# Optimization experiments

Hardware: AMD Instinct MI355X
Metric: run time of the kernel (lower is better)

Reference implementation:

```python
import jax, jax.numpy as jnp
import numpy as np
from jax import lax

B, TX, RX, RATE, DIMZ, HID, DIRS = 8192, 32, 32, 2, 64, 128, 2
S, FEAT = 2 * TX, 2 * TX + 1
BN_EPS = 1e-5
GD_STEP = 1e-6   # hardcoded in original forward
GD_ITERS = 10    # hardcoded in original forward


def setup_inputs() -> dict:
    key = jax.random.key(0)
    ks = jax.random.split(key, 9)
    sc = 1.0 / np.sqrt(HID)
    return {
        "y": jax.random.normal(ks[0], (B, 2 * RX), jnp.float32),
        "H": jax.random.normal(ks[1], (B, 2 * RX, 2 * TX), jnp.float32),
        "x_raw": jax.random.randint(ks[2], (B, 2 * TX, 1), 0, 2 ** RATE).astype(jnp.float32),
        "gru_w_ih": jax.random.uniform(ks[3], (DIRS, 3 * HID, FEAT), jnp.float32, -sc, sc),
        "gru_w_hh": jax.random.uniform(ks[4], (DIRS, 3 * HID, HID), jnp.float32, -sc, sc),
        "gru_b_ih": jax.random.uniform(ks[5], (DIRS, 3 * HID), jnp.float32, -sc, sc),
        "gru_b_hh": jax.random.uniform(ks[6], (DIRS, 3 * HID), jnp.float32, -sc, sc),
        "w_Wz": jax.random.normal(ks[7], (DIMZ, DIRS * HID), jnp.float32),
        "w_Wx": jax.random.normal(ks[8], (DIMZ, DIRS * HID), jnp.float32),
        "bn_gamma": jnp.ones((2 * TX,), jnp.float32),
        "bn_beta": jnp.zeros((2 * TX,), jnp.float32),
        "step_size": 1,
        "iterations": 10,
    }


def _gru_dir(x_seq, wih, whh, bih, bhh):
    # x_seq: (S, B, F); PyTorch GRU cell equations
    xg = jnp.einsum('sbf,gf->sbg', x_seq, wih) + bih  # (S, B, 3H)

    def step(h, xg_t):
        hg = h @ whh.T + bhh
        xr, xz, xn = jnp.split(xg_t, 3, axis=-1)
        hr, hz, hn = jnp.split(hg, 3, axis=-1)
        r = jax.nn.sigmoid(xr + hr)
        z = jax.nn.sigmoid(xz + hz)
        n = jnp.tanh(xn + r * hn)
        h = (1.0 - z) * n + z * h
        return h, h

    h0 = jnp.zeros((x_seq.shape[1], whh.shape[1]), x_seq.dtype)
    _, out = lax.scan(step, h0, xg)
    return out  # (S, B, H)


def reference(y, H, x_raw, gru_w_ih, gru_w_hh, gru_b_ih, gru_b_hh,
              w_Wz, w_Wx, bn_gamma, bn_beta, step_size, iterations):
    # Hty: (B, 2tx, 1), HtH: (B, 2tx, 2tx)
    Hty = jnp.einsum('brt,br->bt', H, y)[..., None]
    HtH = jnp.einsum('brt,bru->btu', H, H)

    # BatchNorm1d over channel dim 2tx (stats over batch and last dim)
    feats = jnp.concatenate([HtH, Hty], axis=-1)  # (B, 2tx, 2tx+1)
    mu = feats.mean(axis=(0, 2), keepdims=True)
    var = feats.var(axis=(0, 2), keepdims=True)
    feats = (feats - mu) / jnp.sqrt(var + BN_EPS)
    feats = feats * bn_gamma[None, :, None] + bn_beta[None, :, None]

    # bidirectional GRU over seq dim (seq_len = 2tx)
    x_seq = jnp.transpose(feats, (1, 0, 2))  # (S, B, F)
    fwd = _gru_dir(x_seq, gru_w_ih[0], gru_w_hh[0], gru_b_ih[0], gru_b_hh[0])
    bwd = _gru_dir(x_seq[::-1], gru_w_ih[1], gru_w_hh[1], gru_b_ih[1], gru_b_hh[1])[::-1]
    go = jnp.concatenate([fwd, bwd], axis=-1)  # (S, B, 2H)

    w_z = jnp.transpose(go @ w_Wz.T, (1, 2, 0))  # (B, dim_z, S)
    w_x = jnp.transpose(go @ w_Wx.T, (1, 0, 2))  # (B, S, dim_z)

    x_hat0 = 2.0 * x_raw - (2.0 ** RATE) + 1.0  # QAM symbols
    z0 = w_z @ x_hat0  # (B, dim_z, 1)

    # gradient-descent loop (step_size/iterations args ignored, as in source)
    wxt = jnp.swapaxes(w_x, 1, 2)        # (B, dim_z, 2tx)
    wxt_hty = wxt @ Hty                  # (B, dim_z, 1)
    whhw = wxt @ (HtH @ w_x)             # (B, dim_z, dim_z)
    two_step = 2.0 * GD_STEP

    def gd(zh, _):
        return zh + two_step * (wxt_hty - whhw @ zh), None

    z_hat, _ = lax.scan(gd, z0, None, length=GD_ITERS)
    return w_x @ z_hat  # (B, 2tx, 1)
```

## Files before the change

### kernel.cpp

```cpp
#include <hip/hip_runtime.h>
#include <math.h>


typedef __attribute__((ext_vector_type(8))) short s8v;
typedef __attribute__((ext_vector_type(4))) float f4v;

__device__ __forceinline__ short f2bf(float x) {
  unsigned u = __float_as_uint(x);
  u += 0x7fffu + ((u >> 16) & 1u);
  return (short)(u >> 16);
}
__device__ __forceinline__ float bf2f(short h) {
  return __uint_as_float(((unsigned)(unsigned short)h) << 16);
}
__device__ __forceinline__ void fma4(float4& c, float a, const float4 w) {
  c.x += a*w.x; c.y += a*w.y; c.z += a*w.z; c.w += a*w.w;
}
__device__ __forceinline__ float vget(const float4& v, int i) { return ((const float*)&v)[i]; }

#define MFMA(A, B, C) __builtin_amdgcn_mfma_f32_16x16x32_bf16((A), (B), (C), 0, 0, 0)

__global__ __launch_bounds__(256) void k_feats(
    const float* __restrict__ Hm, const float* __restrict__ y,
    short* __restrict__ fragX, float* __restrict__ htyU, float* __restrict__ bnacc)
{
  __shared__ __align__(16) float Hl[64][68];
  __shared__ float yl[64];
  __shared__ float s1[64], s2[64];
  const int b = blockIdx.x;
  const int tid = threadIdx.x;
  const float* Hb = Hm + (size_t)b*4096;
  for (int i = tid; i < 4096; i += 256) Hl[i>>6][i&63] = Hb[i];
  if (tid < 64) { yl[tid] = y[b*64+tid]; s1[tid] = 0.f; s2[tid] = 0.f; }
  __syncthreads();

  if (tid < 64) {
    float acc = 0.f;
    for (int r = 0; r < 64; ++r) acc += Hl[r][tid]*yl[r];
    htyU[tid*8192 + b] = acc;
    atomicAdd(&s1[tid], acc);
    atomicAdd(&s2[tid], acc*acc);
  }
  const int tg = tid & 15, ug = tid >> 4;
  float4 acc4[4];
  acc4[0]=acc4[1]=acc4[2]=acc4[3]=make_float4(0.f,0.f,0.f,0.f);
  for (int r = 0; r < 64; ++r) {
    const float4 tv = *(const float4*)&Hl[r][4*tg];
    const float4 uv = *(const float4*)&Hl[r][4*ug];
    #pragma unroll
    for (int tt=0;tt<4;++tt) fma4(acc4[tt], vget(tv,tt), uv);
  }
  const int mt   = (b >> 4) & 3;
  const int brow = b & 15;
  const int u0   = 4*ug;
  short* fbase = fragX + (size_t)(b >> 6)*64*8192
               + (mt*2 + (u0 >> 5))*512 + (brow + 16*((u0 >> 3) & 3))*8 + (u0 & 7);
  #pragma unroll
  for (int tt=0;tt<4;++tt) {
    const int t = 4*tg+tt;
    float sv=0.f, sq=0.f;
    short hib[4], lob[4];
    #pragma unroll
    for (int uu=0;uu<4;++uu) {
      const float v = vget(acc4[tt],uu);
      const short hi = f2bf(v);
      hib[uu] = hi; lob[uu] = f2bf(v - bf2f(hi));
      sv += v; sq += v*v;
    }
    short* dst = fbase + (size_t)t*8192;
    *(short4*)dst          = make_short4(hib[0],hib[1],hib[2],hib[3]);
    *(short4*)(dst + 4096) = make_short4(lob[0],lob[1],lob[2],lob[3]);
    sv += __shfl_down(sv,32); sq += __shfl_down(sq,32);
    sv += __shfl_down(sv,16); sq += __shfl_down(sq,16);
    if ((tid & 63) < 16) { atomicAdd(&s1[t], sv); atomicAdd(&s2[t], sq); }
  }
  __syncthreads();
  if (tid < 64) {
    atomicAdd(&bnacc[tid*16],      s1[tid]);
    atomicAdd(&bnacc[(64+tid)*16], s2[tid]);
  }
}

__global__ void k_bnfin(const float* __restrict__ bnacc, const float* __restrict__ gam,
                        const float* __restrict__ bet, float* __restrict__ bnac)
{
  const int t = threadIdx.x;
  if (t < 64) {
    const float inv = 1.f/532480.f;
    const float mu  = bnacc[t*16]*inv;
    const float var = bnacc[(64+t)*16]*inv - mu*mu;
    const float a = gam[t]*rsqrtf(var + 1e-5f);
    bnac[t] = a;
    bnac[64+t] = bet[t] - mu*a;
  }
}

__global__ __launch_bounds__(256) void k_prep(
    const float* __restrict__ wih, const float* __restrict__ whh,
    const float* __restrict__ Wz, const float* __restrict__ Wx,
    short* __restrict__ Wg, short* __restrict__ W2g, float* __restrict__ rowsum)
{
  const int i = blockIdx.x*256 + threadIdx.x;
  if (i < 294912) {
    const int dd = i / 147456, r = i % 147456;
    const int sp = r / 73728, r2 = r % 73728;
    const int chunk = r2 / 512, e = r2 % 512;
    const int lane = e >> 3, ii = e & 7;
    const int nt = chunk / 6, kt = chunk % 6;
    const int n = nt*16 + (lane & 15);
    const int k = kt*32 + (lane >> 4)*8 + ii;
    const float v = (k < 64) ? wih[dd*24960 + n*65 + k]
                             : whh[dd*49152 + n*128 + (k - 64)];
    const short hi = f2bf(v);
    Wg[i] = sp ? f2bf(v - bf2f(hi)) : hi;
  } else if (i < 360448) {
    const int t = i - 294912;
    const int dd = t / 32768, r = t % 32768;
    const int sp = r / 16384, r2 = r % 16384;
    const int chunk = r2 / 512, e = r2 % 512;
    const int lane = e >> 3, ii = e & 7;
    const int nt2 = chunk / 4, kt = chunk % 4;
    const int n2 = nt2*16 + (lane & 15);
    const int k = kt*32 + (lane >> 4)*8 + ii;
    const float v = (n2 < 64) ? Wx[n2*256 + dd*128 + k]
                              : Wz[(n2 - 64)*256 + dd*128 + k];
    const short hi = f2bf(v);
    W2g[t] = sp ? f2bf(v - bf2f(hi)) : hi;
  } else if (i < 361216) {
    const int t = i - 360448;
    const int dd = t / 384, g = t % 384;
    float ssum = 0.f;
    for (int f = 0; f < 65; ++f) ssum += wih[dd*24960 + g*65 + f];
    rowsum[t] = ssum;
  }
}

__global__ __launch_bounds__(512, 2) void k_scan(
    const short* __restrict__ fragX, const float* __restrict__ htyU,
    const float* __restrict__ xraw,
    const short* __restrict__ Wg, const short* __restrict__ W2g,
    const float* __restrict__ bih, const float* __restrict__ bhh,
    const float* __restrict__ rowsum, const float* __restrict__ bnac,
    const float* __restrict__ wih,
    float* __restrict__ wx_out, float* __restrict__ z0_out)
{
  __shared__ __align__(16) short Ax[8192];
  __shared__ __align__(16) short Ah[16384];

  const int tid = threadIdx.x;
  const int l   = tid & 63;
  const int w   = __builtin_amdgcn_readfirstlane(tid >> 6);
  const int tile = blockIdx.x >> 1, d = blockIdx.x & 1;
  const int b0  = tile * 64;
  const int l15 = l & 15, lq = l >> 4;
  const int j   = 16*w + l15;

  const short* Wgd = Wg  + d*147456;
  const short* W2d = W2g + d*32768;
  float* wxo = wx_out + (size_t)d * (8192ull*4096ull);
  float* z0o = z0_out + (size_t)d * (8192ull*64ull);

  s8v BR[6][2], BZ[6][2], BN[6][2], BP[4][2];
  #pragma unroll
  for (int kt = 0; kt < 6; ++kt)
    #pragma unroll
    for (int sp = 0; sp < 2; ++sp) {
      BR[kt][sp] = *(const s8v*)&Wgd[((sp*24 + w     )*6 + kt)*512 + l*8];
      BZ[kt][sp] = *(const s8v*)&Wgd[((sp*24 + 8 + w )*6 + kt)*512 + l*8];
      BN[kt][sp] = *(const s8v*)&Wgd[((sp*24 + 16 + w)*6 + kt)*512 + l*8];
    }
  #pragma unroll
  for (int kt = 0; kt < 4; ++kt)
    #pragma unroll
    for (int sp = 0; sp < 2; ++sp)
      BP[kt][sp] = *(const s8v*)&W2d[((sp*8 + w)*4 + kt)*512 + l*8];

  const float rsR = rowsum[d*384 + j];
  const float rsZ = rowsum[d*384 + 128 + j];
  const float rsN = rowsum[d*384 + 256 + j];
  const float KR  = bih[d*384 + j]       + bhh[d*384 + j];
  const float KZ  = bih[d*384 + 128 + j] + bhh[d*384 + 128 + j];
  const float KN  = bih[d*384 + 256 + j];
  const float BHN = bhh[d*384 + 256 + j];
  const float w64r = wih[d*24960 + j*65 + 64];
  const float w64z = wih[d*24960 + (128 + j)*65 + 64];
  const float w64n = wih[d*24960 + (256 + j)*65 + 64];

  const int hw_base = (j >> 5)*512 + ((j >> 3) & 3)*128 + (j & 7);

  for (int i = tid; i < 16384; i += 512) Ah[i] = 0;

  f4v hprev[4], z0a[4];
  #pragma unroll
  for (int mt = 0; mt < 4; ++mt) { hprev[mt] = (f4v)0.f; z0a[mt] = (f4v)0.f; }

  {
    const int s0 = d ? 63 : 0;
    const short* src = fragX + (size_t)(tile*64 + s0)*8192;
    *(float4*)((char*)Ax + tid*16)        = *(const float4*)((const char*)src + tid*16);
    *(float4*)((char*)Ax + 8192 + tid*16) = *(const float4*)((const char*)src + 8192 + tid*16);
  }
  __syncthreads();

  for (int it = 0; it < 64; ++it) {
    const int s  = d ? 63 - it : it;
    const int sn = (it < 63) ? (d ? s - 1 : s + 1) : s;

    const short* srcn = fragX + (size_t)(tile*64 + sn)*8192;
    const float4 pf0 = *(const float4*)((const char*)srcn + tid*16);
    const float4 pf1 = *(const float4*)((const char*)srcn + 8192 + tid*16);

    const float a_s = bnac[s], c_s = bnac[64 + s];
    const float crK = c_s*rsR + KR;
    const float czK = c_s*rsZ + KZ;
    const float cnK = c_s*rsN + KN;

    #pragma unroll
    for (int mt = 0; mt < 4; ++mt) {
      f4v Crx = (f4v)0.f, Czx = (f4v)0.f, Cnx = (f4v)0.f;
      f4v Crh = (f4v)0.f, Czh = (f4v)0.f, Cnh = (f4v)0.f;
      #pragma unroll
      for (int kt = 0; kt < 2; ++kt) {
        const s8v axh = *(const s8v*)&Ax[mt*1024 + kt*512 + l*8];
        const s8v axl = *(const s8v*)&Ax[4096 + mt*1024 + kt*512 + l*8];
        Crx = MFMA(axh, BR[kt][0], Crx); Crx = MFMA(axh, BR[kt][1], Crx); Crx = MFMA(axl, BR[kt][0], Crx);
        Czx = MFMA(axh, BZ[kt][0], Czx); Czx = MFMA(axh, BZ[kt][1], Czx); Czx = MFMA(axl, BZ[kt][0], Czx);
        Cnx = MFMA(axh, BN[kt][0], Cnx); Cnx = MFMA(axh, BN[kt][1], Cnx); Cnx = MFMA(axl, BN[kt][0], Cnx);
      }
      #pragma unroll
      for (int kh = 0; kh < 4; ++kh) {
        const s8v ahh = *(const s8v*)&Ah[mt*2048 + kh*512 + l*8];
        const s8v ahl = *(const s8v*)&Ah[8192 + mt*2048 + kh*512 + l*8];
        const int kt = 2 + kh;
        Crh = MFMA(ahh, BR[kt][0], Crh); Crh = MFMA(ahh, BR[kt][1], Crh); Crh = MFMA(ahl, BR[kt][0], Crh);
        Czh = MFMA(ahh, BZ[kt][0], Czh); Czh = MFMA(ahh, BZ[kt][1], Czh); Czh = MFMA(ahl, BZ[kt][0], Czh);
        Cnh = MFMA(ahh, BN[kt][0], Cnh); Cnh = MFMA(ahh, BN[kt][1], Cnh); Cnh = MFMA(ahl, BN[kt][0], Cnh);
      }
      f4v av;
      #pragma unroll
      for (int e = 0; e < 4; ++e) av[e] = htyU[s*8192 + b0 + mt*16 + lq*4 + e];
      Crx += av * w64r; Czx += av * w64z; Cnx += av * w64n;
      #pragma unroll
      for (int e = 0; e < 4; ++e) {
        const float rr  = 1.f/(1.f + __expf(-(a_s*Crx[e] + Crh[e] + crK)));
        const float zz  = 1.f/(1.f + __expf(-(a_s*Czx[e] + Czh[e] + czK)));
        const float pre = a_s*Cnx[e] + cnK + rr*(Cnh[e] + BHN);
        const float ax2 = fabsf(pre);
        const float ee  = __expf(-2.f*ax2);
        const float nn  = copysignf((1.f - ee)/(1.f + ee), pre);
        hprev[mt][e] = (1.f - zz)*nn + zz*hprev[mt][e];
      }
    }
    __syncthreads();

    #pragma unroll
    for (int mt = 0; mt < 4; ++mt)
      #pragma unroll
      for (int e = 0; e < 4; ++e) {
        const float hv = hprev[mt][e];
        const short hi = f2bf(hv);
        const int ad = mt*2048 + hw_base + (lq*4 + e)*8;
        Ah[ad] = hi;
        Ah[8192 + ad] = f2bf(hv - bf2f(hi));
      }
    *(float4*)((char*)Ax + tid*16)        = pf0;
    *(float4*)((char*)Ax + 8192 + tid*16) = pf1;
    __syncthreads();

    #pragma unroll
    for (int mt = 0; mt < 4; ++mt) {
      f4v Cp = (f4v)0.f;
      #pragma unroll
      for (int kt = 0; kt < 4; ++kt) {
        const s8v ahh = *(const s8v*)&Ah[mt*2048 + kt*512 + l*8];
        const s8v ahl = *(const s8v*)&Ah[8192 + mt*2048 + kt*512 + l*8];
        Cp = MFMA(ahh, BP[kt][0], Cp);
        Cp = MFMA(ahh, BP[kt][1], Cp);
        Cp = MFMA(ahl, BP[kt][0], Cp);
      }
      if (w < 4) {
        #pragma unroll
        for (int e = 0; e < 4; ++e)
          wxo[(size_t)(b0 + mt*16 + lq*4 + e)*4096 + s*64 + 16*w + l15] = Cp[e];
      } else {
        f4v xh;
        #pragma unroll
        for (int e = 0; e < 4; ++e)
          xh[e] = 2.f*xraw[(b0 + mt*16 + lq*4 + e)*64 + s] - 3.f;
        z0a[mt] += xh * Cp;
      }
    }
  }
  if (w >= 4) {
    #pragma unroll
    for (int mt = 0; mt < 4; ++mt)
      #pragma unroll
      for (int e = 0; e < 4; ++e)
        z0o[(size_t)(b0 + mt*16 + lq*4 + e)*64 + 16*(w-4) + l15] = z0a[mt][e];
  }
}

__global__ __launch_bounds__(256) void k_gd(
    const float* __restrict__ Hm, const float* __restrict__ y,
    const float* __restrict__ wxf, const float* __restrict__ wxb,
    const float* __restrict__ z0f, const float* __restrict__ z0b,
    float* __restrict__ out)
{
  __shared__ __align__(16) float Hl[64][68];
  __shared__ __align__(16) float wx[64][68];
  __shared__ __align__(16) float tmp[64][68];
  __shared__ float yl[64], wh[64], zv[64];
  const int b = blockIdx.x;
  const int tid = threadIdx.x;
  const float* Hb = Hm + (size_t)b*4096;
  for (int i = tid; i < 4096; i += 256) {
    Hl[i>>6][i&63] = Hb[i];
    wx[i>>6][i&63] = wxf[(size_t)b*4096 + i] + wxb[(size_t)b*4096 + i];
  }
  if (tid < 64) {
    yl[tid] = y[b*64+tid];
    zv[tid] = z0f[(size_t)b*64+tid] + z0b[(size_t)b*64+tid];
  }
  __syncthreads();
  const int zq = tid & 15, tq = tid >> 4;
  #pragma unroll
  for (int rr = 0; rr < 4; ++rr) {
    const int r = 4*tq + rr;
    float4 a = make_float4(0.f,0.f,0.f,0.f);
    for (int t = 0; t < 64; ++t) fma4(a, Hl[r][t], *(const float4*)&wx[t][4*zq]);
    *(float4*)&tmp[r][4*zq] = a;
  }
  __syncthreads();
  float (*ww)[68] = Hl;
  #pragma unroll
  for (int ii = 0; ii < 4; ++ii) {
    const int zi = 4*tq + ii;
    float4 a = make_float4(0.f,0.f,0.f,0.f);
    for (int r = 0; r < 64; ++r) fma4(a, tmp[r][zi], *(const float4*)&tmp[r][4*zq]);
    *(float4*)&ww[zi][4*zq] = a;
  }
  if (tid < 64) {
    float acc = 0.f;
    for (int r = 0; r < 64; ++r) acc += tmp[r][tid]*yl[r];
    wh[tid] = acc;
  }
  __syncthreads();
  for (int itr = 0; itr < 10; ++itr) {
    float nz = 0.f;
    if (tid < 64) {
      float mv = 0.f;
      for (int k2 = 0; k2 < 64; ++k2) mv += ww[tid][k2]*zv[k2];
      nz = zv[tid] + 2e-6f*(wh[tid] - mv);
    }
    __syncthreads();
    if (tid < 64) zv[tid] = nz;
    __syncthreads();
  }
  if (tid < 64) {
    float o = 0.f;
    for (int z2 = 0; z2 < 64; ++z2) o += wx[tid][z2]*zv[z2];
    out[(size_t)b*64 + tid] = o;
  }
}

extern "C" void kernel_launch(void* const* d_in, const int* in_sizes, int n_in,
                              void* d_out, int out_size, void* d_ws, size_t ws_size,
                              hipStream_t stream)
{
  const float* y    = (const float*)d_in[0];
  const float* Hm   = (const float*)d_in[1];
  const float* xraw = (const float*)d_in[2];
  const float* wih  = (const float*)d_in[3];
  const float* whh  = (const float*)d_in[4];
  const float* bih  = (const float*)d_in[5];
  const float* bhh  = (const float*)d_in[6];
  const float* Wz   = (const float*)d_in[7];
  const float* Wx   = (const float*)d_in[8];
  const float* gam  = (const float*)d_in[9];
  const float* bet  = (const float*)d_in[10];
  float* out = (float*)d_out;
  float* ws  = (float*)d_ws;

  float* wxf   = ws;
  float* wxb   = wxf + 33554432ull;
  float* z0f   = wxb + 33554432ull;
  float* z0b   = z0f + 524288ull;
  float* htyU  = z0b + 524288ull;
  float* rows  = htyU + 524288ull;
  float* bnacc = rows + 768ull;
  float* bnac  = bnacc + 2048ull;
  short* Wgs   = (short*)(bnac + 128ull);
  short* W2gs  = Wgs + 294912ull;
  short* fragX = W2gs + 65536ull;

  hipMemsetAsync(bnacc, 0, 2048*sizeof(float), stream);
  k_feats <<<8192, 256, 0, stream>>>(Hm, y, fragX, htyU, bnacc);
  k_prep  <<<1412, 256, 0, stream>>>(wih, whh, Wz, Wx, Wgs, W2gs, rows);
  k_bnfin <<<1, 64, 0, stream>>>(bnacc, gam, bet, bnac);
  k_scan  <<<256, 512, 0, stream>>>(fragX, htyU, xraw, Wgs, W2gs,
                                    bih, bhh, rows, bnac, wih, wxf, z0f);
  k_gd    <<<8192, 256, 0, stream>>>(Hm, y, wxf, wxb, z0f, z0b, out);
}
```

Before: 2.103 ms.

## Double-buffer GRU scan LDS tiles and stage per-step scalars in LDS

Splits the input and hidden-state LDS tiles in the recurrent scan kernel into ping-pong buffers. This removes one of the two block-wide barriers per timestep, since writes to the next step's buffer no longer race with reads of the current one. It also preloads the QAM symbols, the Hty column and the BatchNorm coefficients into LDS once, replacing scattered per-step global loads with vectorised LDS reads. The cost is much more LDS per block (about 131KB), which rules out two resident blocks per CU. With this grid size that may not matter.

```diff
diff --git a/kernel.cpp b/kernel.cpp
--- a/kernel.cpp
+++ b/kernel.cpp
@@ -144,8 +144,11 @@
     const float* __restrict__ wih,
     float* __restrict__ wx_out, float* __restrict__ z0_out)
 {
-  __shared__ __align__(16) short Ax[8192];
-  __shared__ __align__(16) short Ah[16384];
+  __shared__ __align__(16) short Axb[16384];
+  __shared__ __align__(16) short Ahb[32768];
+  __shared__ __align__(16) float xl[64][68];
+  __shared__ __align__(16) float htyl[64][68];
+  __shared__ float bna[128];
 
   const int tid = threadIdx.x;
   const int l   = tid & 63;
@@ -188,7 +191,16 @@
 
   const int hw_base = (j >> 5)*512 + ((j >> 3) & 3)*128 + (j & 7);
 
-  for (int i = tid; i < 16384; i += 512) Ah[i] = 0;
+  for (int i = tid; i < 32768; i += 512) Ahb[i] = 0;
+  for (int i = tid; i < 4096; i += 512) {
+    const int bl = i >> 6, s = i & 63;
+    xl[s][bl] = 2.f*xraw[(size_t)(b0 + bl)*64 + s] - 3.f;
+  }
+  for (int i = tid; i < 4096; i += 512) {
+    const int s = i >> 6, bl = i & 63;
+    htyl[s][bl] = htyU[s*8192 + b0 + bl];
+  }
+  if (tid < 128) bna[tid] = bnac[tid];
 
   f4v hprev[4], z0a[4];
   #pragma unroll
@@ -197,8 +209,8 @@
   {
     const int s0 = d ? 63 : 0;
     const short* src = fragX + (size_t)(tile*64 + s0)*8192;
-    *(float4*)((char*)Ax + tid*16)        = *(const float4*)((const char*)src + tid*16);
-    *(float4*)((char*)Ax + 8192 + tid*16) = *(const float4*)((const char*)src + 8192 + tid*16);
+    *(float4*)((char*)Axb + tid*16)        = *(const float4*)((const char*)src + tid*16);
+    *(float4*)((char*)Axb + 8192 + tid*16) = *(const float4*)((const char*)src + 8192 + tid*16);
   }
   __syncthreads();
 
@@ -206,11 +218,16 @@
     const int s  = d ? 63 - it : it;
     const int sn = (it < 63) ? (d ? s - 1 : s + 1) : s;
 
+    short* AxR = Axb + ((it & 1) << 13);
+    short* AxW = Axb + (((it + 1) & 1) << 13);
+    short* AhR = Ahb + (((it + 1) & 1) << 14);
+    short* AhW = Ahb + ((it & 1) << 14);
+
     const short* srcn = fragX + (size_t)(tile*64 + sn)*8192;
     const float4 pf0 = *(const float4*)((const char*)srcn + tid*16);
     const float4 pf1 = *(const float4*)((const char*)srcn + 8192 + tid*16);
 
-    const float a_s = bnac[s], c_s = bnac[64 + s];
+    const float a_s = bna[s], c_s = bna[64 + s];
     const float crK = c_s*rsR + KR;
     const float czK = c_s*rsZ + KZ;
     const float cnK = c_s*rsN + KN;
@@ -221,24 +238,23 @@
       f4v Crh = (f4v)0.f, Czh = (f4v)0.f, Cnh = (f4v)0.f;
       #pragma unroll
       for (int kt = 0; kt < 2; ++kt) {
-        const s8v axh = *(const s8v*)&Ax[mt*1024 + kt*512 + l*8];
-        const s8v axl = *(const s8v*)&Ax[4096 + mt*1024 + kt*512 + l*8];
+        const s8v axh = *(const s8v*)&AxR[mt*1024 + kt*512 + l*8];
+        const s8v axl = *(const s8v*)&AxR[4096 + mt*1024 + kt*512 + l*8];
         Crx = MFMA(axh, BR[kt][0], Crx); Crx = MFMA(axh, BR[kt][1], Crx); Crx = MFMA(axl, BR[kt][0], Crx);
         Czx = MFMA(axh, BZ[kt][0], Czx); Czx = MFMA(axh, BZ[kt][1], Czx); Czx = MFMA(axl, BZ[kt][0], Czx);
         Cnx = MFMA(axh, BN[kt][0], Cnx); Cnx = MFMA(axh, BN[kt][1], Cnx); Cnx = MFMA(axl, BN[kt][0], Cnx);
       }
       #pragma unroll
       for (int kh = 0; kh < 4; ++kh) {
-        const s8v ahh = *(const s8v*)&Ah[mt*2048 + kh*512 + l*8];
-        const s8v ahl = *(const s8v*)&Ah[8192 + mt*2048 + kh*512 + l*8];
+        const s8v ahh = *(const s8v*)&AhR[mt*2048 + kh*512 + l*8];
+        const s8v ahl = *(const s8v*)&AhR[8192 + mt*2048 + kh*512 + l*8];
         const int kt = 2 + kh;
         Crh = MFMA(ahh, BR[kt][0], Crh); Crh = MFMA(ahh, BR[kt][1], Crh); Crh = MFMA(ahl, BR[kt][0], Crh);
         Czh = MFMA(ahh, BZ[kt][0], Czh); Czh = MFMA(ahh, BZ[kt][1], Czh); Czh = MFMA(ahl, BZ[kt][0], Czh);
         Cnh = MFMA(ahh, BN[kt][0], Cnh); Cnh = MFMA(ahh, BN[kt][1], Cnh); Cnh = MFMA(ahl, BN[kt][0], Cnh);
       }
-      f4v av;
-      #pragma unroll
-      for (int e = 0; e < 4; ++e) av[e] = htyU[s*8192 + b0 + mt*16 + lq*4 + e];
+      const float4 av4 = *(const float4*)&htyl[s][mt*16 + lq*4];
+      f4v av; av[0]=av4.x; av[1]=av4.y; av[2]=av4.z; av[3]=av4.w;
       Crx += av * w64r; Czx += av * w64z; Cnx += av * w64n;
       #pragma unroll
       for (int e = 0; e < 4; ++e) {
@@ -251,7 +267,6 @@
         hprev[mt][e] = (1.f - zz)*nn + zz*hprev[mt][e];
       }
     }
-    __syncthreads();
 
     #pragma unroll
     for (int mt = 0; mt < 4; ++mt)
@@ -260,11 +275,11 @@
         const float hv = hprev[mt][e];
         const short hi = f2bf(hv);
         const int ad = mt*2048 + hw_base + (lq*4 + e)*8;
-        Ah[ad] = hi;
-        Ah[8192 + ad] = f2bf(hv - bf2f(hi));
-      }
-    *(float4*)((char*)Ax + tid*16)        = pf0;
-    *(float4*)((char*)Ax + 8192 + tid*16) = pf1;
+        AhW[ad] = hi;
+        AhW[8192 + ad] = f2bf(hv - bf2f(hi));
+      }
+    *(float4*)((char*)AxW + tid*16)        = pf0;
+    *(float4*)((char*)AxW + 8192 + tid*16) = pf1;
     __syncthreads();
 
     #pragma unroll
@@ -272,8 +287,8 @@
       f4v Cp = (f4v)0.f;
       #pragma unroll
       for (int kt = 0; kt < 4; ++kt) {
-        const s8v ahh = *(const s8v*)&Ah[mt*2048 + kt*512 + l*8];
-        const s8v ahl = *(const s8v*)&Ah[8192 + mt*2048 + kt*512 + l*8];
+        const s8v ahh = *(const s8v*)&AhW[mt*2048 + kt*512 + l*8];
+        const s8v ahl = *(const s8v*)&AhW[8192 + mt*2048 + kt*512 + l*8];
         Cp = MFMA(ahh, BP[kt][0], Cp);
         Cp = MFMA(ahh, BP[kt][1], Cp);
         Cp = MFMA(ahl, BP[kt][0], Cp);
@@ -283,10 +298,8 @@
         for (int e = 0; e < 4; ++e)
           wxo[(size_t)(b0 + mt*16 + lq*4 + e)*4096 + s*64 + 16*w + l15] = Cp[e];
       } else {
-        f4v xh;
-        #pragma unroll
-        for (int e = 0; e < 4; ++e)
-          xh[e] = 2.f*xraw[(b0 + mt*16 + lq*4 + e)*64 + s] - 3.f;
+        const float4 xh4 = *(const float4*)&xl[s][mt*16 + lq*4];
+        f4v xh; xh[0]=xh4.x; xh[1]=xh4.y; xh[2]=xh4.z; xh[3]=xh4.w;
         z0a[mt] += xh * Cp;
       }
     }
```

Measured after the change: 2.051 ms. 2.5% less time.
